# Optimization experiments

Hardware: AMD Instinct MI355X
Metric: run time of the kernel (lower is better)

Reference implementation:

```python
import jax, jax.numpy as jnp
import numpy as np

MAX_FRAMES = 12
TOPK = 49
NUM_SAMPLES = 256
SIGMA = 0.05
LN_EPS = 1e-5


def setup_inputs() -> dict:
    key = jax.random.key(0)
    ks = jax.random.split(key, 6)
    B, MF, N, D = 8, MAX_FRAMES, 197, 512
    x = jax.random.normal(ks[0], (B, MF * N, D), dtype=jnp.float32)
    noise = jax.random.normal(ks[1], (B * MF, NUM_SAMPLES, N - 1), dtype=jnp.float32)
    ln_gamma = jnp.ones((D,), jnp.float32)
    ln_beta = jnp.zeros((D,), jnp.float32)
    w_in = jax.random.normal(ks[2], (D, D // 2), dtype=jnp.float32) * 0.02
    w1 = jax.random.normal(ks[3], (D, D // 2), dtype=jnp.float32) * 0.02
    w2 = jax.random.normal(ks[4], (D // 2, 1), dtype=jnp.float32) * 0.02
    return {"x": x, "noise": noise, "ln_gamma": ln_gamma, "ln_beta": ln_beta,
            "w_in": w_in, "w1": w1, "w2": w2}


def reference(x, noise, ln_gamma, ln_beta, w_in, w1, w2):
    B, L, D = x.shape
    N = L // MAX_FRAMES
    xf = x.reshape(B * MAX_FRAMES, N, D)          # (b, N, D)

    # PredictorLG: LayerNorm -> Linear -> GELU (torch GELU is exact erf)
    mu = xf.mean(-1, keepdims=True)
    var = xf.var(-1, keepdims=True)               # biased, matches torch LayerNorm
    hn = (xf - mu) * jax.lax.rsqrt(var + LN_EPS) * ln_gamma + ln_beta
    h = jax.nn.gelu(hn @ w_in, approximate=False)  # (b, N, D/2)
    # concat local features with broadcast global (cls-token) features
    g = jnp.broadcast_to(h[:, :1, :], h.shape)
    cat = jnp.concatenate([h, g], axis=-1)         # (b, N, D)
    score = jnp.tanh(jax.nn.gelu(cat @ w1, approximate=False) @ w2)[..., 0]  # (b, N)

    sp = score[:, 1:]                              # (b, d) spatial scores, d = N-1
    b_eff, ns, d = noise.shape
    pert = sp[:, None, :] + noise * SIGMA          # (b, ns, d)

    # top-k set per sample; sorted ascending (matches torch sort of topk indices)
    order = jnp.argsort(-pert, axis=-1)            # descending by value
    top_sorted = jnp.sort(order[..., :TOPK], axis=-1)  # (b, ns, k)

    # mean of one-hots == scatter-add counts / num_samples (avoids one-hot blowup)
    bi = jnp.arange(b_eff)[:, None, None]
    pos = jnp.arange(TOPK)[None, None, :]
    ind = jnp.zeros((b_eff, TOPK, d), x.dtype).at[bi, pos, top_sorted].add(1.0) / ns

    cls_feat = xf[:, :1, :]                        # (b, 1, D)
    spat_feat = xf[:, 1:, :]                       # (b, d, D)
    sel = jnp.einsum('bkl,bld->bkd', ind, spat_feat)  # (b, k, D)
    out = jnp.concatenate([cls_feat, sel], axis=1)    # (b, 1+k, D)
    return out.reshape(B, MAX_FRAMES * (1 + TOPK), D)
```

## Files before the change

### kernel.cpp

```cpp
#include <hip/hip_runtime.h>
#include <math.h>

#define NFRAME 96
#define NTOK   197
#define NSPAT  196
#define DIM    512
#define DH     256
#define NSAMP  256
#define KSEL   49
#define SIG    0.05f
#define MPAD   208
#define MTOT   (NFRAME * MPAD)

typedef unsigned short u16;
typedef __attribute__((ext_vector_type(8))) short bf16x8;
typedef __attribute__((ext_vector_type(4))) float f32x4;

__device__ __forceinline__ float gelu_exact(float v) {
    return 0.5f * v * (1.0f + erff(v * 0.70710678118654752440f));
}
__device__ __forceinline__ unsigned bf16_rne(float f) {
    unsigned u = __float_as_uint(f);
    return (u + 0x7fffu + ((u >> 16) & 1u)) >> 16;
}
__device__ __forceinline__ float bf16_to_f(unsigned h) {
    return __uint_as_float(h << 16);
}

__global__ __launch_bounds__(256) void k0_prep(
    const float* __restrict__ x, const float* __restrict__ gamma,
    const float* __restrict__ beta,
    const float* __restrict__ w_in, const float* __restrict__ w1,
    u16* __restrict__ wiT_hi, u16* __restrict__ wiT_lo,
    u16* __restrict__ w1T_hi, u16* __restrict__ w1T_lo,
    u16* __restrict__ xs_hi, u16* __restrict__ xs_lo)
{
    if (blockIdx.x < 512) {
        const int n = blockIdx.x & 255, which = blockIdx.x >> 8;
        const float* w = which ? w1 : w_in;
        u16* th = which ? w1T_hi : wiT_hi;
        u16* tl = which ? w1T_lo : wiT_lo;
        for (int k = threadIdx.x; k < DIM; k += 256) {
            float v = w[(size_t)k * DH + n];
            unsigned hi = bf16_rne(v);
            unsigned lo = bf16_rne(v - bf16_to_f(hi));
            th[(size_t)n * DIM + k] = (u16)hi;
            tl[(size_t)n * DIM + k] = (u16)lo;
        }
        return;
    }
    const int row  = (blockIdx.x - 512) * 4 + (threadIdx.x >> 6);
    const int lane = threadIdx.x & 63;
    const int f = row / MPAD;
    int rr = row - f * MPAD; if (rr > NTOK - 1) rr = NTOK - 1;
    const float* xr = x + ((size_t)f * NTOK + rr) * DIM + lane * 8;
    float4 a = *(const float4*)xr, b4 = *(const float4*)(xr + 4);
    float e[8] = {a.x, a.y, a.z, a.w, b4.x, b4.y, b4.z, b4.w};
    float s = 0.f, sq = 0.f;
    #pragma unroll
    for (int j = 0; j < 8; ++j) { s += e[j]; sq += e[j] * e[j]; }
    #pragma unroll
    for (int o = 32; o > 0; o >>= 1) {
        s  += __shfl_xor(s,  o, 64);
        sq += __shfl_xor(sq, o, 64);
    }
    const float mu  = s * (1.f / 512.f);
    const float var = sq * (1.f / 512.f) - mu * mu;
    const float rs  = 1.f / sqrtf(var + 1e-5f);

    const float* gp = gamma + lane * 8;
    const float* bp = beta + lane * 8;
    float4 g0 = *(const float4*)gp, g1 = *(const float4*)(gp + 4);
    float4 b0 = *(const float4*)bp, b1 = *(const float4*)(bp + 4);
    float gg[8] = {g0.x, g0.y, g0.z, g0.w, g1.x, g1.y, g1.z, g1.w};
    float bt[8] = {b0.x, b0.y, b0.z, b0.w, b1.x, b1.y, b1.z, b1.w};

    unsigned hw[4], lw[4];
    #pragma unroll
    for (int p = 0; p < 4; ++p) {
        float s0 = rs * gg[2*p],   s1 = rs * gg[2*p+1];
        float v0 = e[2*p]   * s0 + (bt[2*p]   - mu * s0);
        float v1 = e[2*p+1] * s1 + (bt[2*p+1] - mu * s1);
        unsigned h0 = bf16_rne(v0), h1 = bf16_rne(v1);
        float l0 = v0 - bf16_to_f(h0), l1 = v1 - bf16_to_f(h1);
        hw[p] = h0 | (h1 << 16);
        lw[p] = bf16_rne(l0) | (bf16_rne(l1) << 16);
    }
    size_t off = (size_t)row * DIM + lane * 8;
    *(uint4*)(xs_hi + off) = make_uint4(hw[0], hw[1], hw[2], hw[3]);
    *(uint4*)(xs_lo + off) = make_uint4(lw[0], lw[1], lw[2], lw[3]);
}

#define LDG 72
__global__ __launch_bounds__(256, 2) void k1_gemm1(
    const u16* __restrict__ xs_hi, const u16* __restrict__ xs_lo,
    const u16* __restrict__ wiT_hi, const u16* __restrict__ wiT_lo,
    u16* __restrict__ h_hi, u16* __restrict__ h_lo)
{
    __shared__ u16 Ah[2][64][LDG], Al[2][64][LDG], Bh[2][64][LDG], Bl[2][64][LDG];
    const int t = threadIdx.x, lane = t & 63, wv = t >> 6;
    const int linear = (blockIdx.x & 7) * 156 + (blockIdx.x >> 3);
    const int Mb = linear >> 2, Nb = linear & 3;
    const int R0 = Mb * 64, N0 = Nb * 64;
    const int wm = wv >> 1, wn = wv & 1;
    const int m15 = lane & 15, q = lane >> 4;

    f32x4 acc[2][2];
    #pragma unroll
    for (int i = 0; i < 2; ++i)
        #pragma unroll
        for (int j = 0; j < 2; ++j)
            acc[i][j] = (f32x4){0.f, 0.f, 0.f, 0.f};

    const int ar = t >> 2, as = (t & 3) * 16;
    const size_t abase = (size_t)(R0 + ar) * DIM + as;
    const size_t bbase = (size_t)(N0 + ar) * DIM + as;

    uint4 pAh0 = *(const uint4*)(xs_hi + abase);
    uint4 pAh1 = *(const uint4*)(xs_hi + abase + 8);
    uint4 pAl0 = *(const uint4*)(xs_lo + abase);
    uint4 pAl1 = *(const uint4*)(xs_lo + abase + 8);
    uint4 pBh0 = *(const uint4*)(wiT_hi + bbase);
    uint4 pBh1 = *(const uint4*)(wiT_hi + bbase + 8);
    uint4 pBl0 = *(const uint4*)(wiT_lo + bbase);
    uint4 pBl1 = *(const uint4*)(wiT_lo + bbase + 8);

    for (int k0 = 0; k0 < DIM; k0 += 64) {
        const int p = (k0 >> 6) & 1;
        *(uint4*)&Ah[p][ar][as]     = pAh0;
        *(uint4*)&Ah[p][ar][as + 8] = pAh1;
        *(uint4*)&Al[p][ar][as]     = pAl0;
        *(uint4*)&Al[p][ar][as + 8] = pAl1;
        *(uint4*)&Bh[p][ar][as]     = pBh0;
        *(uint4*)&Bh[p][ar][as + 8] = pBh1;
        *(uint4*)&Bl[p][ar][as]     = pBl0;
        *(uint4*)&Bl[p][ar][as + 8] = pBl1;
        if (k0 + 64 < DIM) {
            pAh0 = *(const uint4*)(xs_hi + abase + k0 + 64);
            pAh1 = *(const uint4*)(xs_hi + abase + k0 + 72);
            pAl0 = *(const uint4*)(xs_lo + abase + k0 + 64);
            pAl1 = *(const uint4*)(xs_lo + abase + k0 + 72);
            pBh0 = *(const uint4*)(wiT_hi + bbase + k0 + 64);
            pBh1 = *(const uint4*)(wiT_hi + bbase + k0 + 72);
            pBl0 = *(const uint4*)(wiT_lo + bbase + k0 + 64);
            pBl1 = *(const uint4*)(wiT_lo + bbase + k0 + 72);
        }
        __syncthreads();

        #pragma unroll
        for (int kh = 0; kh < 2; ++kh) {
            const int ko = kh * 32 + q * 8;
            bf16x8 ah[2], al[2], bh[2], bl[2];
            #pragma unroll
            for (int i = 0; i < 2; ++i) {
                ah[i] = *(const bf16x8*)&Ah[p][wm*32 + i*16 + m15][ko];
                al[i] = *(const bf16x8*)&Al[p][wm*32 + i*16 + m15][ko];
                bh[i] = *(const bf16x8*)&Bh[p][wn*32 + i*16 + m15][ko];
                bl[i] = *(const bf16x8*)&Bl[p][wn*32 + i*16 + m15][ko];
            }
            #pragma unroll
            for (int mt = 0; mt < 2; ++mt)
                #pragma unroll
                for (int nt = 0; nt < 2; ++nt) {
                    f32x4 c = acc[mt][nt];
                    c = __builtin_amdgcn_mfma_f32_16x16x32_bf16(ah[mt], bh[nt], c, 0, 0, 0);
                    c = __builtin_amdgcn_mfma_f32_16x16x32_bf16(al[mt], bh[nt], c, 0, 0, 0);
                    c = __builtin_amdgcn_mfma_f32_16x16x32_bf16(ah[mt], bl[nt], c, 0, 0, 0);
                    acc[mt][nt] = c;
                }
        }
    }

    #pragma unroll
    for (int mt = 0; mt < 2; ++mt)
        #pragma unroll
        for (int nt = 0; nt < 2; ++nt)
            #pragma unroll
            for (int reg = 0; reg < 4; ++reg) {
                int r = R0 + wm*32 + mt*16 + q*4 + reg;
                int c = N0 + wn*32 + nt*16 + m15;
                float v = gelu_exact(acc[mt][nt][reg]);
                unsigned hb = bf16_rne(v);
                unsigned lb = bf16_rne(v - bf16_to_f(hb));
                size_t off = (size_t)r * DH + c;
                h_hi[off] = (u16)hb;
                h_lo[off] = (u16)lb;
            }
}

__global__ __launch_bounds__(256) void k1g_gbias(
    const u16* __restrict__ h_hi, const u16* __restrict__ h_lo,
    const u16* __restrict__ w1T_hi, const u16* __restrict__ w1T_lo,
    float* __restrict__ gbias)
{
    const int f = blockIdx.x, n = threadIdx.x;
    const size_t hoff = (size_t)f * MPAD * DH;
    const size_t woff = (size_t)n * DIM + DH;
    float s = 0.f;
    for (int k = 0; k < DH; k += 8) {
        uint4 vh = *(const uint4*)(h_hi + hoff + k);
        uint4 vl = *(const uint4*)(h_lo + hoff + k);
        uint4 uh = *(const uint4*)(w1T_hi + woff + k);
        uint4 ul = *(const uint4*)(w1T_lo + woff + k);
        const unsigned* ph = (const unsigned*)&vh;
        const unsigned* pl = (const unsigned*)&vl;
        const unsigned* qh = (const unsigned*)&uh;
        const unsigned* ql = (const unsigned*)&ul;
        #pragma unroll
        for (int w = 0; w < 4; ++w) {
            float a0 = bf16_to_f(ph[w] & 0xffffu) + bf16_to_f(pl[w] & 0xffffu);
            float a1 = bf16_to_f(ph[w] >> 16)     + bf16_to_f(pl[w] >> 16);
            float b0 = bf16_to_f(qh[w] & 0xffffu) + bf16_to_f(ql[w] & 0xffffu);
            float b1 = bf16_to_f(qh[w] >> 16)     + bf16_to_f(ql[w] >> 16);
            s += a0 * b0 + a1 * b1;
        }
    }
    gbias[f * DH + n] = s;
}

__global__ __launch_bounds__(256, 2) void k1_gemm2(
    const u16* __restrict__ h_hi, const u16* __restrict__ h_lo,
    const u16* __restrict__ w1T_hi, const u16* __restrict__ w1T_lo,
    const float* __restrict__ w2, const float* __restrict__ gbias,
    float* __restrict__ s_quar)
{
    __shared__ u16 Ah[2][64][LDG], Al[2][64][LDG], Bh[2][64][LDG], Bl[2][64][LDG];
    __shared__ float red[2][2][32];
    const int t = threadIdx.x, lane = t & 63, wv = t >> 6;
    const int linear = (blockIdx.x & 7) * 156 + (blockIdx.x >> 3);
    const int Mb = linear >> 2, Nb = linear & 3;
    const int R0 = Mb * 64, N0 = Nb * 64;
    const int wm = wv >> 1, wn = wv & 1;
    const int m15 = lane & 15, q = lane >> 4;

    f32x4 acc[2][2];
    #pragma unroll
    for (int i = 0; i < 2; ++i)
        #pragma unroll
        for (int j = 0; j < 2; ++j)
            acc[i][j] = (f32x4){0.f, 0.f, 0.f, 0.f};

    const int ar = t >> 2, as = (t & 3) * 16;
    const size_t abase = (size_t)(R0 + ar) * DH + as;
    const size_t bbase = (size_t)(N0 + ar) * DIM + as;

    uint4 pAh0 = *(const uint4*)(h_hi + abase);
    uint4 pAh1 = *(const uint4*)(h_hi + abase + 8);
    uint4 pAl0 = *(const uint4*)(h_lo + abase);
    uint4 pAl1 = *(const uint4*)(h_lo + abase + 8);
    uint4 pBh0 = *(const uint4*)(w1T_hi + bbase);
    uint4 pBh1 = *(const uint4*)(w1T_hi + bbase + 8);
    uint4 pBl0 = *(const uint4*)(w1T_lo + bbase);
    uint4 pBl1 = *(const uint4*)(w1T_lo + bbase + 8);

    for (int k0 = 0; k0 < DH; k0 += 64) {
        const int p = (k0 >> 6) & 1;
        *(uint4*)&Ah[p][ar][as]     = pAh0;
        *(uint4*)&Ah[p][ar][as + 8] = pAh1;
        *(uint4*)&Al[p][ar][as]     = pAl0;
        *(uint4*)&Al[p][ar][as + 8] = pAl1;
        *(uint4*)&Bh[p][ar][as]     = pBh0;
        *(uint4*)&Bh[p][ar][as + 8] = pBh1;
        *(uint4*)&Bl[p][ar][as]     = pBl0;
        *(uint4*)&Bl[p][ar][as + 8] = pBl1;
        if (k0 + 64 < DH) {
            pAh0 = *(const uint4*)(h_hi + abase + k0 + 64);
            pAh1 = *(const uint4*)(h_hi + abase + k0 + 72);
            pAl0 = *(const uint4*)(h_lo + abase + k0 + 64);
            pAl1 = *(const uint4*)(h_lo + abase + k0 + 72);
            pBh0 = *(const uint4*)(w1T_hi + bbase + k0 + 64);
            pBh1 = *(const uint4*)(w1T_hi + bbase + k0 + 72);
            pBl0 = *(const uint4*)(w1T_lo + bbase + k0 + 64);
            pBl1 = *(const uint4*)(w1T_lo + bbase + k0 + 72);
        }
        __syncthreads();

        #pragma unroll
        for (int kh = 0; kh < 2; ++kh) {
            const int ko = kh * 32 + q * 8;
            bf16x8 ah[2], al[2], bh[2], bl[2];
            #pragma unroll
            for (int i = 0; i < 2; ++i) {
                ah[i] = *(const bf16x8*)&Ah[p][wm*32 + i*16 + m15][ko];
                al[i] = *(const bf16x8*)&Al[p][wm*32 + i*16 + m15][ko];
                bh[i] = *(const bf16x8*)&Bh[p][wn*32 + i*16 + m15][ko];
                bl[i] = *(const bf16x8*)&Bl[p][wn*32 + i*16 + m15][ko];
            }
            #pragma unroll
            for (int mt = 0; mt < 2; ++mt)
                #pragma unroll
                for (int nt = 0; nt < 2; ++nt) {
                    f32x4 c = acc[mt][nt];
                    c = __builtin_amdgcn_mfma_f32_16x16x32_bf16(ah[mt], bh[nt], c, 0, 0, 0);
                    c = __builtin_amdgcn_mfma_f32_16x16x32_bf16(al[mt], bh[nt], c, 0, 0, 0);
                    c = __builtin_amdgcn_mfma_f32_16x16x32_bf16(ah[mt], bl[nt], c, 0, 0, 0);
                    acc[mt][nt] = c;
                }
        }
    }

    float w2v[2];
    int   cIdx[2];
    #pragma unroll
    for (int nt = 0; nt < 2; ++nt) {
        cIdx[nt] = N0 + wn*32 + nt*16 + m15;
        w2v[nt]  = w2[cIdx[nt]];
    }
    #pragma unroll
    for (int mt = 0; mt < 2; ++mt)
        #pragma unroll
        for (int reg = 0; reg < 4; ++reg) {
            int r = R0 + wm*32 + mt*16 + q*4 + reg;
            int f = r / MPAD;
            float gb0 = gbias[f * DH + cIdx[0]];
            float gb1 = gbias[f * DH + cIdx[1]];
            float s = gelu_exact(acc[mt][0][reg] + gb0) * w2v[0] +
                      gelu_exact(acc[mt][1][reg] + gb1) * w2v[1];
            #pragma unroll
            for (int o = 1; o <= 8; o <<= 1)
                s += __shfl_xor(s, o, 64);
            if (m15 == 0)
                red[wn][wm][mt*16 + q*4 + reg] = s;
        }
    __syncthreads();
    if (t < 64) {
        int wmj = t >> 5, rl = t & 31;
        float sv = red[0][wmj][rl] + red[1][wmj][rl];
        s_quar[(size_t)Nb * MTOT + R0 + t] = sv;
    }
}

__global__ __launch_bounds__(1024) void k2_select(
    const float* __restrict__ s_quar, const float* __restrict__ noise,
    int* __restrict__ hist2)
{
    const int fb   = blockIdx.x;
    const int f    = fb >> 1;
    const int half = fb & 1;
    const int t    = threadIdx.x;
    const int lane = t & 63;
    const int wv   = t >> 6;

    __shared__ int hist_s[KSEL * NSPAT];
    for (int i = t; i < KSEL * NSPAT; i += 1024) hist_s[i] = 0;

    const float* s0 = s_quar;
    const float* s1 = s_quar + MTOT;
    const float* s2 = s_quar + 2 * (size_t)MTOT;
    const float* s3 = s_quar + 3 * (size_t)MTOT;
    float spv[4];
    #pragma unroll
    for (int j = 0; j < 4; ++j) {
        int l = lane + 64 * j;
        if (l < NSPAT) {
            size_t idx = (size_t)f * MPAD + 1 + l;
            spv[j] = tanhf(s0[idx] + s1[idx] + s2[idx] + s3[idx]);
        } else spv[j] = 0.f;
    }
    __syncthreads();

    const unsigned long long lmask = (1ull << lane) - 1ull;

    for (int si = 0; si < 8; ++si) {
        const int s = half * 128 + wv * 8 + si;
        const float* nz = noise + ((size_t)f * NSAMP + s) * NSPAT;
        unsigned key[4];
        #pragma unroll
        for (int j = 0; j < 4; ++j) {
            int l = lane + 64 * j;
            if (l < NSPAT) {
                float p = spv[j] + nz[l] * SIG;
                unsigned u = __float_as_uint(p);
                key[j] = (u & 0x80000000u) ? ~u : (u | 0x80000000u);
            } else {
                key[j] = 0u;
            }
        }

        unsigned ans;
        {
            int c31 = 0;
            #pragma unroll
            for (int j = 0; j < 4; ++j)
                c31 += __popcll(__ballot(key[j] >= 0x80000000u));
            ans = (c31 >= KSEL) ? 0x80000000u : 0x40000000u;
        }
        for (int bit = 29; bit >= 0; --bit) {
            unsigned cand = ans | (1u << bit);
            int cnt = 0;
            #pragma unroll
            for (int j = 0; j < 4; ++j)
                cnt += __popcll(__ballot(key[j] >= cand));
            if (cnt >= KSEL) ans = cand;
        }

        unsigned long long eq[4];
        int cgt = 0;
        #pragma unroll
        for (int j = 0; j < 4; ++j) {
            cgt += __popcll(__ballot(key[j] > ans));
            eq[j] = __ballot(key[j] == ans);
        }
        const int quota = KSEL - cgt;
        int eqpre[4]; { int run = 0;
            #pragma unroll
            for (int j = 0; j < 4; ++j) { eqpre[j] = run; run += __popcll(eq[j]); } }

        int pre = 0;
        #pragma unroll
        for (int j = 0; j < 4; ++j) {
            bool iseq = (key[j] == ans);
            int trk = eqpre[j] + __popcll(eq[j] & lmask);
            bool selj = (key[j] > ans) || (iseq && trk < quota);
            unsigned long long sb = __ballot(selj);
            int rk = pre + __popcll(sb & lmask);
            if (selj)
                atomicAdd(&hist_s[rk * NSPAT + lane + 64 * j], 1);
            pre += __popcll(sb);
        }
    }

    __syncthreads();
    int* hb = hist2 + (size_t)fb * (KSEL * NSPAT);
    for (int i = t; i < KSEL * NSPAT; i += 1024)
        hb[i] = hist_s[i];
}

#define KP3 52
__global__ __launch_bounds__(256) void k3_output(
    const float* __restrict__ x, const int* __restrict__ hist2,
    float* __restrict__ out)
{
    const int b   = blockIdx.x >> 3;
    const int ds  = blockIdx.x & 7;
    const int d0  = ds * 64;
    const int t   = threadIdx.x;
    const int tdc = t & 15;
    const int tk  = t >> 4;

    __shared__ float hist_s[NSPAT * KP3 + 16];

    const int* h0 = hist2 + (size_t)(2 * b) * (KSEL * NSPAT);
    const int* h1 = h0 + KSEL * NSPAT;
    for (int i = t; i < KSEL * NSPAT; i += 256) {
        int k = i / NSPAT;
        int l = i - k * NSPAT;
        hist_s[l * KP3 + k] = (float)(h0[i] + h1[i]);
    }
    for (int i = t; i < NSPAT * 3 + 16; i += 256) {
        int l = i / 3, j = i - l * 3;
        int idx = (i < NSPAT * 3) ? (l * KP3 + KSEL + j) : (NSPAT * KP3 + i - NSPAT * 3);
        hist_s[idx] = 0.f;
    }
    if (t < 64)
        out[(size_t)b * 50 * DIM + d0 + t] = x[(size_t)b * NTOK * DIM + d0 + t];
    __syncthreads();

    const float* xs = x + ((size_t)b * NTOK + 1) * DIM + d0 + tdc * 4;
    float4 acc[4];
    #pragma unroll
    for (int i = 0; i < 4; ++i) acc[i] = make_float4(0.f, 0.f, 0.f, 0.f);

    #pragma unroll 7
    for (int l = 0; l < NSPAT; ++l) {
        float4 v  = *(const float4*)(xs + (size_t)l * DIM);
        float4 w4 = *(const float4*)&hist_s[l * KP3 + tk * 4];
        acc[0].x += w4.x * v.x; acc[0].y += w4.x * v.y;
        acc[0].z += w4.x * v.z; acc[0].w += w4.x * v.w;
        acc[1].x += w4.y * v.x; acc[1].y += w4.y * v.y;
        acc[1].z += w4.y * v.z; acc[1].w += w4.y * v.w;
        acc[2].x += w4.z * v.x; acc[2].y += w4.z * v.y;
        acc[2].z += w4.z * v.z; acc[2].w += w4.z * v.w;
        acc[3].x += w4.w * v.x; acc[3].y += w4.w * v.y;
        acc[3].z += w4.w * v.z; acc[3].w += w4.w * v.w;
    }

    const float inv = 1.f / 256.f;
    #pragma unroll
    for (int i = 0; i < 4; ++i) {
        int k = tk * 4 + i;
        if (k < KSEL) {
            float4 o = make_float4(acc[i].x * inv, acc[i].y * inv,
                                   acc[i].z * inv, acc[i].w * inv);
            *(float4*)&out[((size_t)b * 50 + 1 + k) * DIM + d0 + tdc * 4] = o;
        }
    }
}

extern "C" void kernel_launch(void* const* d_in, const int* in_sizes, int n_in,
                              void* d_out, int out_size, void* d_ws, size_t ws_size,
                              hipStream_t stream)
{
    const float* x     = (const float*)d_in[0];
    const float* noise = (const float*)d_in[1];
    const float* gamma = (const float*)d_in[2];
    const float* beta  = (const float*)d_in[3];
    const float* w_in  = (const float*)d_in[4];
    const float* w1    = (const float*)d_in[5];
    const float* w2    = (const float*)d_in[6];
    float* out = (float*)d_out;

    char* ws = (char*)d_ws;
    int*   hist2   = (int*)  (ws + 0);
    float* gbias   = (float*)(ws + 0);
    float* s_quar  = (float*)(ws + 7375872);
    u16*   wiT_hi  = (u16*)  (ws + 7695360);
    u16*   wiT_lo  = (u16*)  (ws + 7957504);
    u16*   w1T_hi  = (u16*)  (ws + 8219648);
    u16*   w1T_lo  = (u16*)  (ws + 8481792);
    u16*   h_hi    = (u16*)  (ws + 8743936);
    u16*   h_lo    = (u16*)  (ws + 18967552);
    u16*   xs_hi   = (u16*)  (ws + 29191168);
    u16*   xs_lo   = (u16*)  (ws + 49638400);

    k0_prep<<<512 + MTOT / 4, 256, 0, stream>>>(x, gamma, beta, w_in, w1,
                                                wiT_hi, wiT_lo, w1T_hi, w1T_lo,
                                                xs_hi, xs_lo);
    k1_gemm1<<<(MTOT / 64) * 4, 256, 0, stream>>>(xs_hi, xs_lo, wiT_hi, wiT_lo,
                                                  h_hi, h_lo);
    k1g_gbias<<<NFRAME, 256, 0, stream>>>(h_hi, h_lo, w1T_hi, w1T_lo, gbias);
    k1_gemm2<<<(MTOT / 64) * 4, 256, 0, stream>>>(h_hi, h_lo, w1T_hi, w1T_lo,
                                                  w2, gbias, s_quar);
    k2_select<<<NFRAME * 2, 1024, 0, stream>>>(s_quar, noise, hist2);
    k3_output<<<NFRAME * 8, 256, 0, stream>>>(x, hist2, out);
}
```

Baseline: 221.4 us.

## Use direct global-to-LDS loads with XOR swizzle and 128-row tiles in GEMMs

```diff
diff --git a/kernel.cpp b/kernel.cpp
--- a/kernel.cpp
+++ b/kernel.cpp
@@ -25,6 +25,15 @@
 }
 __device__ __forceinline__ float bf16_to_f(unsigned h) {
     return __uint_as_float(h << 16);
+}
+
+__device__ __forceinline__ void gld16(const u16* g, u16* l) {
+    __builtin_amdgcn_global_load_lds(
+        (const __attribute__((address_space(1))) void*)g,
+        (__attribute__((address_space(3))) void*)l, 16, 0, 0);
+}
+__device__ __forceinline__ bf16x8 srd(const u16* base, int r, int cw) {
+    return *(const bf16x8*)((const char*)base + r * 128 + (((cw) ^ (r & 7)) << 4));
 }
 
 __global__ __launch_bounds__(256) void k0_prep(
@@ -91,93 +100,82 @@
     *(uint4*)(xs_lo + off) = make_uint4(lw[0], lw[1], lw[2], lw[3]);
 }
 
-#define LDG 72
-__global__ __launch_bounds__(256, 2) void k1_gemm1(
+__global__ __launch_bounds__(256, 3) void k1_gemm1(
     const u16* __restrict__ xs_hi, const u16* __restrict__ xs_lo,
     const u16* __restrict__ wiT_hi, const u16* __restrict__ wiT_lo,
     u16* __restrict__ h_hi, u16* __restrict__ h_lo)
 {
-    __shared__ u16 Ah[2][64][LDG], Al[2][64][LDG], Bh[2][64][LDG], Bl[2][64][LDG];
+    __shared__ u16 Ah[128][64], Al[128][64], Bh[64][64], Bl[64][64];
     const int t = threadIdx.x, lane = t & 63, wv = t >> 6;
-    const int linear = (blockIdx.x & 7) * 156 + (blockIdx.x >> 3);
+    const int linear = (blockIdx.x & 7) * 78 + (blockIdx.x >> 3);
     const int Mb = linear >> 2, Nb = linear & 3;
-    const int R0 = Mb * 64, N0 = Nb * 64;
+    const int R0 = Mb * 128, N0 = Nb * 64;
     const int wm = wv >> 1, wn = wv & 1;
     const int m15 = lane & 15, q = lane >> 4;
-
-    f32x4 acc[2][2];
-    #pragma unroll
-    for (int i = 0; i < 2; ++i)
+    const int r8 = lane >> 3;
+    const int cg = (lane & 7) ^ r8;
+
+    f32x4 acc[4][2];
+    #pragma unroll
+    for (int i = 0; i < 4; ++i)
         #pragma unroll
         for (int j = 0; j < 2; ++j)
             acc[i][j] = (f32x4){0.f, 0.f, 0.f, 0.f};
 
-    const int ar = t >> 2, as = (t & 3) * 16;
-    const size_t abase = (size_t)(R0 + ar) * DIM + as;
-    const size_t bbase = (size_t)(N0 + ar) * DIM + as;
-
-    uint4 pAh0 = *(const uint4*)(xs_hi + abase);
-    uint4 pAh1 = *(const uint4*)(xs_hi + abase + 8);
-    uint4 pAl0 = *(const uint4*)(xs_lo + abase);
-    uint4 pAl1 = *(const uint4*)(xs_lo + abase + 8);
-    uint4 pBh0 = *(const uint4*)(wiT_hi + bbase);
-    uint4 pBh1 = *(const uint4*)(wiT_hi + bbase + 8);
-    uint4 pBl0 = *(const uint4*)(wiT_lo + bbase);
-    uint4 pBl1 = *(const uint4*)(wiT_lo + bbase + 8);
-
     for (int k0 = 0; k0 < DIM; k0 += 64) {
-        const int p = (k0 >> 6) & 1;
-        *(uint4*)&Ah[p][ar][as]     = pAh0;
-        *(uint4*)&Ah[p][ar][as + 8] = pAh1;
-        *(uint4*)&Al[p][ar][as]     = pAl0;
-        *(uint4*)&Al[p][ar][as + 8] = pAl1;
-        *(uint4*)&Bh[p][ar][as]     = pBh0;
-        *(uint4*)&Bh[p][ar][as + 8] = pBh1;
-        *(uint4*)&Bl[p][ar][as]     = pBl0;
-        *(uint4*)&Bl[p][ar][as + 8] = pBl1;
-        if (k0 + 64 < DIM) {
-            pAh0 = *(const uint4*)(xs_hi + abase + k0 + 64);
-            pAh1 = *(const uint4*)(xs_hi + abase + k0 + 72);
-            pAl0 = *(const uint4*)(xs_lo + abase + k0 + 64);
-            pAl1 = *(const uint4*)(xs_lo + abase + k0 + 72);
-            pBh0 = *(const uint4*)(wiT_hi + bbase + k0 + 64);
-            pBh1 = *(const uint4*)(wiT_hi + bbase + k0 + 72);
-            pBl0 = *(const uint4*)(wiT_lo + bbase + k0 + 64);
-            pBl1 = *(const uint4*)(wiT_lo + bbase + k0 + 72);
-        }
         __syncthreads();
+        #pragma unroll
+        for (int j = 0; j < 4; ++j) {
+            const int rA = wv * 32 + j * 8;
+            const size_t src = (size_t)(R0 + rA + r8) * DIM + k0 + cg * 8;
+            gld16(xs_hi + src, &Ah[rA][0]);
+            gld16(xs_lo + src, &Al[rA][0]);
+        }
+        #pragma unroll
+        for (int j = 0; j < 2; ++j) {
+            const int rB = wv * 16 + j * 8;
+            const size_t src = (size_t)(N0 + rB + r8) * DIM + k0 + cg * 8;
+            gld16(wiT_hi + src, &Bh[rB][0]);
+            gld16(wiT_lo + src, &Bl[rB][0]);
+        }
+        __syncthreads();
 
         #pragma unroll
         for (int kh = 0; kh < 2; ++kh) {
-            const int ko = kh * 32 + q * 8;
-            bf16x8 ah[2], al[2], bh[2], bl[2];
-            #pragma unroll
-            for (int i = 0; i < 2; ++i) {
-                ah[i] = *(const bf16x8*)&Ah[p][wm*32 + i*16 + m15][ko];
-                al[i] = *(const bf16x8*)&Al[p][wm*32 + i*16 + m15][ko];
-                bh[i] = *(const bf16x8*)&Bh[p][wn*32 + i*16 + m15][ko];
-                bl[i] = *(const bf16x8*)&Bl[p][wn*32 + i*16 + m15][ko];
+            const int cw = kh * 4 + q;
+            bf16x8 a_h[4], a_l[4], b_h[2], b_l[2];
+            #pragma unroll
+            for (int i = 0; i < 4; ++i) {
+                const int r = wm * 64 + i * 16 + m15;
+                a_h[i] = srd(&Ah[0][0], r, cw);
+                a_l[i] = srd(&Al[0][0], r, cw);
             }
             #pragma unroll
-            for (int mt = 0; mt < 2; ++mt)
+            for (int n = 0; n < 2; ++n) {
+                const int r = wn * 32 + n * 16 + m15;
+                b_h[n] = srd(&Bh[0][0], r, cw);
+                b_l[n] = srd(&Bl[0][0], r, cw);
+            }
+            #pragma unroll
+            for (int mt = 0; mt < 4; ++mt)
                 #pragma unroll
                 for (int nt = 0; nt < 2; ++nt) {
                     f32x4 c = acc[mt][nt];
-                    c = __builtin_amdgcn_mfma_f32_16x16x32_bf16(ah[mt], bh[nt], c, 0, 0, 0);
-                    c = __builtin_amdgcn_mfma_f32_16x16x32_bf16(al[mt], bh[nt], c, 0, 0, 0);
-                    c = __builtin_amdgcn_mfma_f32_16x16x32_bf16(ah[mt], bl[nt], c, 0, 0, 0);
+                    c = __builtin_amdgcn_mfma_f32_16x16x32_bf16(a_h[mt], b_h[nt], c, 0, 0, 0);
+                    c = __builtin_amdgcn_mfma_f32_16x16x32_bf16(a_l[mt], b_h[nt], c, 0, 0, 0);
+                    c = __builtin_amdgcn_mfma_f32_16x16x32_bf16(a_h[mt], b_l[nt], c, 0, 0, 0);
                     acc[mt][nt] = c;
                 }
         }
     }
 
     #pragma unroll
-    for (int mt = 0; mt < 2; ++mt)
+    for (int mt = 0; mt < 4; ++mt)
         #pragma unroll
         for (int nt = 0; nt < 2; ++nt)
             #pragma unroll
             for (int reg = 0; reg < 4; ++reg) {
-                int r = R0 + wm*32 + mt*16 + q*4 + reg;
+                int r = R0 + wm*64 + mt*16 + q*4 + reg;
                 int c = N0 + wn*32 + nt*16 + m15;
                 float v = gelu_exact(acc[mt][nt][reg]);
                 unsigned hb = bf16_rne(v);
@@ -218,82 +216,72 @@
     gbias[f * DH + n] = s;
 }
 
-__global__ __launch_bounds__(256, 2) void k1_gemm2(
+__global__ __launch_bounds__(256, 3) void k1_gemm2(
     const u16* __restrict__ h_hi, const u16* __restrict__ h_lo,
     const u16* __restrict__ w1T_hi, const u16* __restrict__ w1T_lo,
     const float* __restrict__ w2, const float* __restrict__ gbias,
     float* __restrict__ s_quar)
 {
-    __shared__ u16 Ah[2][64][LDG], Al[2][64][LDG], Bh[2][64][LDG], Bl[2][64][LDG];
-    __shared__ float red[2][2][32];
+    __shared__ u16 Ah[128][64], Al[128][64], Bh[64][64], Bl[64][64];
+    __shared__ float red[2][2][64];
     const int t = threadIdx.x, lane = t & 63, wv = t >> 6;
-    const int linear = (blockIdx.x & 7) * 156 + (blockIdx.x >> 3);
+    const int linear = (blockIdx.x & 7) * 78 + (blockIdx.x >> 3);
     const int Mb = linear >> 2, Nb = linear & 3;
-    const int R0 = Mb * 64, N0 = Nb * 64;
+    const int R0 = Mb * 128, N0 = Nb * 64;
     const int wm = wv >> 1, wn = wv & 1;
     const int m15 = lane & 15, q = lane >> 4;
-
-    f32x4 acc[2][2];
-    #pragma unroll
-    for (int i = 0; i < 2; ++i)
+    const int r8 = lane >> 3;
+    const int cg = (lane & 7) ^ r8;
+
+    f32x4 acc[4][2];
+    #pragma unroll
+    for (int i = 0; i < 4; ++i)
         #pragma unroll
         for (int j = 0; j < 2; ++j)
             acc[i][j] = (f32x4){0.f, 0.f, 0.f, 0.f};
 
-    const int ar = t >> 2, as = (t & 3) * 16;
-    const size_t abase = (size_t)(R0 + ar) * DH + as;
-    const size_t bbase = (size_t)(N0 + ar) * DIM + as;
-
-    uint4 pAh0 = *(const uint4*)(h_hi + abase);
-    uint4 pAh1 = *(const uint4*)(h_hi + abase + 8);
-    uint4 pAl0 = *(const uint4*)(h_lo + abase);
-    uint4 pAl1 = *(const uint4*)(h_lo + abase + 8);
-    uint4 pBh0 = *(const uint4*)(w1T_hi + bbase);
-    uint4 pBh1 = *(const uint4*)(w1T_hi + bbase + 8);
-    uint4 pBl0 = *(const uint4*)(w1T_lo + bbase);
-    uint4 pBl1 = *(const uint4*)(w1T_lo + bbase + 8);
-
     for (int k0 = 0; k0 < DH; k0 += 64) {
-        const int p = (k0 >> 6) & 1;
-        *(uint4*)&Ah[p][ar][as]     = pAh0;
-        *(uint4*)&Ah[p][ar][as + 8] = pAh1;
-        *(uint4*)&Al[p][ar][as]     = pAl0;
-        *(uint4*)&Al[p][ar][as + 8] = pAl1;
-        *(uint4*)&Bh[p][ar][as]     = pBh0;
-        *(uint4*)&Bh[p][ar][as + 8] = pBh1;
-        *(uint4*)&Bl[p][ar][as]     = pBl0;
-        *(uint4*)&Bl[p][ar][as + 8] = pBl1;
-        if (k0 + 64 < DH) {
-            pAh0 = *(const uint4*)(h_hi + abase + k0 + 64);
-            pAh1 = *(const uint4*)(h_hi + abase + k0 + 72);
-            pAl0 = *(const uint4*)(h_lo + abase + k0 + 64);
-            pAl1 = *(const uint4*)(h_lo + abase + k0 + 72);
-            pBh0 = *(const uint4*)(w1T_hi + bbase + k0 + 64);
-            pBh1 = *(const uint4*)(w1T_hi + bbase + k0 + 72);
-            pBl0 = *(const uint4*)(w1T_lo + bbase + k0 + 64);
-            pBl1 = *(const uint4*)(w1T_lo + bbase + k0 + 72);
-        }
         __syncthreads();
+        #pragma unroll
+        for (int j = 0; j < 4; ++j) {
+            const int rA = wv * 32 + j * 8;
+            const size_t src = (size_t)(R0 + rA + r8) * DH + k0 + cg * 8;
+            gld16(h_hi + src, &Ah[rA][0]);
+            gld16(h_lo + src, &Al[rA][0]);
+        }
+        #pragma unroll
+        for (int j = 0; j < 2; ++j) {
+            const int rB = wv * 16 + j * 8;
+            const size_t src = (size_t)(N0 + rB + r8) * DIM + k0 + cg * 8;
+            gld16(w1T_hi + src, &Bh[rB][0]);
+            gld16(w1T_lo + src, &Bl[rB][0]);
+        }
+        __syncthreads();
 
         #pragma unroll
         for (int kh = 0; kh < 2; ++kh) {
-            const int ko = kh * 32 + q * 8;
-            bf16x8 ah[2], al[2], bh[2], bl[2];
-            #pragma unroll
-            for (int i = 0; i < 2; ++i) {
-                ah[i] = *(const bf16x8*)&Ah[p][wm*32 + i*16 + m15][ko];
-                al[i] = *(const bf16x8*)&Al[p][wm*32 + i*16 + m15][ko];
-                bh[i] = *(const bf16x8*)&Bh[p][wn*32 + i*16 + m15][ko];
-                bl[i] = *(const bf16x8*)&Bl[p][wn*32 + i*16 + m15][ko];
+            const int cw = kh * 4 + q;
+            bf16x8 a_h[4], a_l[4], b_h[2], b_l[2];
+            #pragma unroll
+            for (int i = 0; i < 4; ++i) {
+                const int r = wm * 64 + i * 16 + m15;
+                a_h[i] = srd(&Ah[0][0], r, cw);
+                a_l[i] = srd(&Al[0][0], r, cw);
             }
             #pragma unroll
-            for (int mt = 0; mt < 2; ++mt)
+            for (int n = 0; n < 2; ++n) {
+                const int r = wn * 32 + n * 16 + m15;
+                b_h[n] = srd(&Bh[0][0], r, cw);
+                b_l[n] = srd(&Bl[0][0], r, cw);
+            }
+            #pragma unroll
+            for (int mt = 0; mt < 4; ++mt)
                 #pragma unroll
                 for (int nt = 0; nt < 2; ++nt) {
                     f32x4 c = acc[mt][nt];
-                    c = __builtin_amdgcn_mfma_f32_16x16x32_bf16(ah[mt], bh[nt], c, 0, 0, 0);
-                    c = __builtin_amdgcn_mfma_f32_16x16x32_bf16(al[mt], bh[nt], c, 0, 0, 0);
-                    c = __builtin_amdgcn_mfma_f32_16x16x32_bf16(ah[mt], bl[nt], c, 0, 0, 0);
+                    c = __builtin_amdgcn_mfma_f32_16x16x32_bf16(a_h[mt], b_h[nt], c, 0, 0, 0);
+                    c = __builtin_amdgcn_mfma_f32_16x16x32_bf16(a_l[mt], b_h[nt], c, 0, 0, 0);
+                    c = __builtin_amdgcn_mfma_f32_16x16x32_bf16(a_h[mt], b_l[nt], c, 0, 0, 0);
                     acc[mt][nt] = c;
                 }
         }
@@ -307,10 +295,10 @@
         w2v[nt]  = w2[cIdx[nt]];
     }
     #pragma unroll
-    for (int mt = 0; mt < 2; ++mt)
+    for (int mt = 0; mt < 4; ++mt)
         #pragma unroll
         for (int reg = 0; reg < 4; ++reg) {
-            int r = R0 + wm*32 + mt*16 + q*4 + reg;
+            int r = R0 + wm*64 + mt*16 + q*4 + reg;
             int f = r / MPAD;
             float gb0 = gbias[f * DH + cIdx[0]];
             float gb1 = gbias[f * DH + cIdx[1]];
@@ -323,8 +311,8 @@
                 red[wn][wm][mt*16 + q*4 + reg] = s;
         }
     __syncthreads();
-    if (t < 64) {
-        int wmj = t >> 5, rl = t & 31;
+    if (t < 128) {
+        int wmj = t >> 6, rl = t & 63;
         float sv = red[0][wmj][rl] + red[1][wmj][rl];
         s_quar[(size_t)Nb * MTOT + R0 + t] = sv;
     }
@@ -516,11 +504,11 @@
     k0_prep<<<512 + MTOT / 4, 256, 0, stream>>>(x, gamma, beta, w_in, w1,
                                                 wiT_hi, wiT_lo, w1T_hi, w1T_lo,
                                                 xs_hi, xs_lo);
-    k1_gemm1<<<(MTOT / 64) * 4, 256, 0, stream>>>(xs_hi, xs_lo, wiT_hi, wiT_lo,
-                                                  h_hi, h_lo);
+    k1_gemm1<<<(MTOT / 128) * 4, 256, 0, stream>>>(xs_hi, xs_lo, wiT_hi, wiT_lo,
+                                                   h_hi, h_lo);
     k1g_gbias<<<NFRAME, 256, 0, stream>>>(h_hi, h_lo, w1T_hi, w1T_lo, gbias);
-    k1_gemm2<<<(MTOT / 64) * 4, 256, 0, stream>>>(h_hi, h_lo, w1T_hi, w1T_lo,
-                                                  w2, gbias, s_quar);
+    k1_gemm2<<<(MTOT / 128) * 4, 256, 0, stream>>>(h_hi, h_lo, w1T_hi, w1T_lo,
+                                                   w2, gbias, s_quar);
     k2_select<<<NFRAME * 2, 1024, 0, stream>>>(s_quar, noise, hist2);
     k3_output<<<NFRAME * 8, 256, 0, stream>>>(x, hist2, out);
 }
```

Result: faster. 214.2 us (-3.3%).
